# Kernel tuning notes

Measured on AMD Instinct MI355X. Metric: run time of the kernel, lower is better.

The kernel has to match this reference:

```python
import jax, jax.numpy as jnp
import numpy as np
from jax.scipy.special import logsumexp

B, S, L = 256, 512, 128


def setup_inputs() -> dict:
    key = jax.random.key(0)
    k1, k2, k3, k4, k5 = jax.random.split(key, 5)
    inputs = jax.random.normal(k1, (B, S, L), dtype=jnp.float32)
    labels = jax.random.randint(k2, (B, S), 0, L, dtype=jnp.int64)
    mask = jnp.ones((B, S), dtype=bool)
    # xavier_normal for (L, L): std = sqrt(2 / (L + L))
    transitions = jax.random.normal(k3, (L, L), dtype=jnp.float32) * np.sqrt(2.0 / (2 * L))
    start_transitions = jax.random.normal(k4, (L,), dtype=jnp.float32)
    end_transitions = jax.random.normal(k5, (L,), dtype=jnp.float32)
    return {
        "inputs": inputs,
        "labels": labels,
        "mask": mask,
        "transitions": transitions,
        "start_transitions": start_transitions,
        "end_transitions": end_transitions,
    }


def _input_likelihood(logits, transitions, start_t, end_t, mask):
    # logits: [B,S,L], mask: [B,S] bool -> logZ: [B]
    logits_t = jnp.swapaxes(logits, 0, 1)  # [S,B,L]
    mask_t = jnp.swapaxes(mask, 0, 1)      # [S,B]
    alpha0 = start_t[None, :] + logits_t[0]  # [B,L]

    def step(alpha, xs):
        emit, m = xs  # emit: [B,L], m: [B]
        # inner[b, i, j] = alpha[b,i] + emit[b,j] + T[i,j]
        inner = alpha[:, :, None] + emit[:, None, :] + transitions[None, :, :]
        new_alpha = logsumexp(inner, axis=1)  # [B,L]
        alpha = jnp.where(m[:, None], new_alpha, alpha)
        return alpha, None

    alpha, _ = jax.lax.scan(step, alpha0, (logits_t[1:], mask_t[1:]))
    stops = alpha + end_t[None, :]
    return logsumexp(stops, axis=-1)  # [B]


def _joint_likelihood(logits, transitions, start_t, end_t, tags, mask):
    # logits: [B,S,L], tags/mask: [B,S] -> score: [B]
    b, s, l = logits.shape
    maskf = mask.astype(logits.dtype)
    score = start_t[tags[:, 0]]  # [B]
    # transition scores for i = 0..S-2, gated by mask[:, i+1]
    trans_sc = transitions[tags[:, :-1], tags[:, 1:]] * maskf[:, 1:]  # [B,S-1]
    # emit scores at positions 0..S-2, gated by mask[:, i]
    emit_all = jnp.take_along_axis(logits, tags[:, :, None], axis=2)[:, :, 0]  # [B,S]
    emit_sc = emit_all[:, :-1] * maskf[:, :-1]
    score = score + trans_sc.sum(axis=1) + emit_sc.sum(axis=1)
    # last valid tag per sequence
    last_idx = mask.sum(axis=1).astype(jnp.int32) - 1  # [B]
    last_tags = jnp.take_along_axis(tags, last_idx[:, None], axis=1)[:, 0]  # [B]
    score = score + end_t[last_tags]
    last_input_sc = jnp.take_along_axis(logits[:, -1, :], last_tags[:, None], axis=1)[:, 0]
    score = score + last_input_sc * maskf[:, -1]
    return score


def reference(inputs, labels, mask, transitions, start_transitions, end_transitions):
    log_denominator = _input_likelihood(inputs, transitions, start_transitions, end_transitions, mask)
    log_numerator = _joint_likelihood(inputs, transitions, start_transitions, end_transitions, labels, mask)
    return jnp.sum(log_numerator - log_denominator)
```

## Files before the change

### kernel.cpp

```cpp
#include <hip/hip_runtime.h>
#include <hip/hip_bf16.h>

#define BB 256
#define SS 512
#define LL 128
#define MB 16
#define NCH 16
#define NSCAN (2 * NCH * 16)
#define CST 16
#define WUP 8

typedef __attribute__((ext_vector_type(8))) short bf16x8;
typedef __attribute__((ext_vector_type(4))) float f32x4;

__device__ __forceinline__ unsigned short f2bf(float x) {
    __hip_bfloat16 h = __float2bfloat16(x);
    return *reinterpret_cast<unsigned short*>(&h);
}
__device__ __forceinline__ float bf2f_lo(unsigned u) { return __uint_as_float(u << 16); }
__device__ __forceinline__ float wave_sum(float v) {
    #pragma unroll
    for (int off = 32; off > 0; off >>= 1)
        v += __shfl_xor(v, off);
    return v;
}
__device__ __forceinline__ unsigned umax2(unsigned a, unsigned b) { return a > b ? a : b; }
__device__ __forceinline__ unsigned packbf(float lo, float hi) {
    unsigned ua = __float_as_uint(hi) + 0x8000u;
    unsigned ub = __float_as_uint(lo) + 0x8000u;
    return __builtin_amdgcn_perm(ua, ub, 0x07060302u);
}

template<int DIR>
__device__ __forceinline__ void scan_dir(
    const float* __restrict__ lg,
    const float* __restrict__ trans,
    const float* __restrict__ bnd,
    const int ci, const int gb, const bool exact,
    const int w, const int q, const int r15,
    unsigned short (*e_lds)[MB][136],
    float* __restrict__ vF, float* __restrict__ wB,
    float* __restrict__ fsA, float* __restrict__ feA, int* __restrict__ sigA)
{
    const int snap_t  = (DIR == 1) ? CST * ci : 511 - CST * ci;
    const int t_begin = exact ? ((DIR == 1) ? 1 : 510) : (snap_t - (WUP - 1) * DIR);
    const int tinit   = t_begin - DIR;
    const int nwarm   = exact ? 0 : WUP;
    const int nmeas   = (ci == NCH - 1) ? (CST - 1) : CST;

    bf16x8 afrag[2][4];
    #pragma unroll
    for (int nt = 0; nt < 2; ++nt) {
        const int j = (w << 5) + nt * 16 + r15;
        #pragma unroll
        for (int kt = 0; kt < 4; ++kt) {
            const int k0 = kt * 32 + (q << 3);
            bf16x8 f;
            #pragma unroll
            for (int i = 0; i < 8; ++i) {
                const int k = k0 + i;
                const float tv = (DIR == 1) ? trans[k * LL + j] : trans[j * LL + k];
                ((unsigned short*)&f)[i] = f2bf(__expf(tv));
            }
            afrag[nt][kt] = f;
        }
    }

    bf16x8 bfrag[4];
    #pragma unroll
    for (int kt = 0; kt < 4; ++kt) {
        const int k0 = kt * 32 + (q << 3);
        bf16x8 f;
        #pragma unroll
        for (int i = 0; i < 8; ++i) {
            const int k = k0 + i;
            const float lv = lg[(size_t)tinit * LL + k];
            ((unsigned short*)&f)[i] = f2bf(__expf(exact ? (bnd[k] + lv) : lv));
        }
        bfrag[kt] = f;
    }

    const float* empf = lg + (w << 5) + (q << 2);
    auto ld2 = [&](int t, float4& a, float4& b) {
        int tp = t;
        tp = tp < 0 ? 0 : (tp > 511 ? 511 : tp);
        a = *(const float4*)(empf + (size_t)tp * LL);
        b = *(const float4*)(empf + (size_t)tp * LL + 16);
    };

    float4 e0a, e0b, e1a, e1b, e2a, e2b, e3a, e3b;
    ld2(t_begin,           e0a, e0b);
    ld2(t_begin + 1 * DIR, e1a, e1b);
    ld2(t_begin + 2 * DIR, e2a, e2b);
    ld2(t_begin + 3 * DIR, e3a, e3b);

    float scale_now = 1.0f, scale_nxt = 1.0f;
    int   pend_now  = 0,    pend_nxt  = 0;
    int   cexp      = 0;

    auto frag_sum = [&]() -> float {
        float s = 0.f;
        #pragma unroll
        for (int kt = 0; kt < 4; ++kt) {
            const unsigned short* pp = (const unsigned short*)&bfrag[kt];
            #pragma unroll
            for (int i = 0; i < 8; ++i)
                s += bf2f_lo((unsigned)pp[i]);
        }
        s += __shfl_xor(s, 16);
        s += __shfl_xor(s, 32);
        return s;
    };

    auto body = [&](int t, float4& ea, float4& eb) {
        float esc[8];
        esc[0] = scale_now * __expf(ea.x);
        esc[1] = scale_now * __expf(ea.y);
        esc[2] = scale_now * __expf(ea.z);
        esc[3] = scale_now * __expf(ea.w);
        esc[4] = scale_now * __expf(eb.x);
        esc[5] = scale_now * __expf(eb.y);
        esc[6] = scale_now * __expf(eb.z);
        esc[7] = scale_now * __expf(eb.w);
        f32x4 a0a = {0,0,0,0}, a0b = {0,0,0,0}, a1a = {0,0,0,0}, a1b = {0,0,0,0};
        a0a = __builtin_amdgcn_mfma_f32_16x16x32_bf16(afrag[0][0], bfrag[0], a0a, 0, 0, 0);
        a0b = __builtin_amdgcn_mfma_f32_16x16x32_bf16(afrag[0][1], bfrag[1], a0b, 0, 0, 0);
        a1a = __builtin_amdgcn_mfma_f32_16x16x32_bf16(afrag[1][0], bfrag[0], a1a, 0, 0, 0);
        a1b = __builtin_amdgcn_mfma_f32_16x16x32_bf16(afrag[1][1], bfrag[1], a1b, 0, 0, 0);
        a0a = __builtin_amdgcn_mfma_f32_16x16x32_bf16(afrag[0][2], bfrag[2], a0a, 0, 0, 0);
        a0b = __builtin_amdgcn_mfma_f32_16x16x32_bf16(afrag[0][3], bfrag[3], a0b, 0, 0, 0);
        a1a = __builtin_amdgcn_mfma_f32_16x16x32_bf16(afrag[1][2], bfrag[2], a1a, 0, 0, 0);
        a1b = __builtin_amdgcn_mfma_f32_16x16x32_bf16(afrag[1][3], bfrag[3], a1b, 0, 0, 0);
        cexp += pend_now;
        ld2(t + 4 * DIR, ea, eb);
        unsigned p[4];
        p[0] = packbf((a0a[0] + a0b[0]) * esc[0], (a0a[1] + a0b[1]) * esc[1]);
        p[1] = packbf((a0a[2] + a0b[2]) * esc[2], (a0a[3] + a0b[3]) * esc[3]);
        p[2] = packbf((a1a[0] + a1b[0]) * esc[4], (a1a[1] + a1b[1]) * esc[5]);
        p[3] = packbf((a1a[2] + a1b[2]) * esc[6], (a1a[3] + a1b[3]) * esc[7]);
        const int buf = t & 1;
        *(uint2*)&e_lds[buf][r15][(w << 5) + (q << 2)]      = make_uint2(p[0], p[1]);
        *(uint2*)&e_lds[buf][r15][(w << 5) + 16 + (q << 2)] = make_uint2(p[2], p[3]);
        asm volatile("s_waitcnt lgkmcnt(0)" ::: "memory");
        __builtin_amdgcn_s_barrier();
        asm volatile("" ::: "memory");
        unsigned um = 0u;
        #pragma unroll
        for (int kt = 0; kt < 4; ++kt) {
            bfrag[kt] = *(const bf16x8*)&e_lds[buf][r15][kt * 32 + (q << 3)];
            const unsigned* pu = (const unsigned*)&bfrag[kt];
            um = umax2(umax2(umax2(um, pu[0]), pu[1]), umax2(pu[2], pu[3]));
        }
        um = umax2(um, (unsigned)__shfl_xor((int)um, 16));
        um = umax2(um, (unsigned)__shfl_xor((int)um, 32));
        const int ke = (int)((um >> 23) & 0xff);
        scale_now = scale_nxt;
        pend_now  = pend_nxt;
        scale_nxt = __int_as_float((254 - ke) << 23);
        pend_nxt  = ke - 127;
    };

    int t = t_begin;
    for (int n = 0; n < nwarm; n += 4) {
        body(t,           e0a, e0b);
        body(t + 1 * DIR, e1a, e1b);
        body(t + 2 * DIR, e2a, e2b);
        body(t + 3 * DIR, e3a, e3b);
        t += 4 * DIR;
    }

    const float fs_val = frag_sum();
    cexp = 0;

    const int nm4 = nmeas & ~3;
    for (int n = 0; n < nm4; n += 4) {
        body(t,           e0a, e0b);
        body(t + 1 * DIR, e1a, e1b);
        body(t + 2 * DIR, e2a, e2b);
        body(t + 3 * DIR, e3a, e3b);
        t += 4 * DIR;
    }
    if (nm4 < nmeas) {
        body(t,           e0a, e0b);
        body(t + 1 * DIR, e1a, e1b);
        body(t + 2 * DIR, e2a, e2b);
    }

    const float fe_val = frag_sum();

    if (DIR == 1) {
        if (ci == NCH - 1 && w == 0) {
            #pragma unroll
            for (int kt = 0; kt < 4; ++kt) {
                const unsigned short* pp = (const unsigned short*)&bfrag[kt];
                float4 o0, o1;
                o0.x = bf2f_lo((unsigned)pp[0]); o0.y = bf2f_lo((unsigned)pp[1]);
                o0.z = bf2f_lo((unsigned)pp[2]); o0.w = bf2f_lo((unsigned)pp[3]);
                o1.x = bf2f_lo((unsigned)pp[4]); o1.y = bf2f_lo((unsigned)pp[5]);
                o1.z = bf2f_lo((unsigned)pp[6]); o1.w = bf2f_lo((unsigned)pp[7]);
                *(float4*)&vF[(size_t)gb * LL + kt * 32 + (q << 3)]     = o0;
                *(float4*)&vF[(size_t)gb * LL + kt * 32 + (q << 3) + 4] = o1;
            }
        }
    } else if (ci == NCH - 1) {
        f32x4 a0a = {0,0,0,0}, a0b = {0,0,0,0}, a1a = {0,0,0,0}, a1b = {0,0,0,0};
        a0a = __builtin_amdgcn_mfma_f32_16x16x32_bf16(afrag[0][0], bfrag[0], a0a, 0, 0, 0);
        a0b = __builtin_amdgcn_mfma_f32_16x16x32_bf16(afrag[0][1], bfrag[1], a0b, 0, 0, 0);
        a1a = __builtin_amdgcn_mfma_f32_16x16x32_bf16(afrag[1][0], bfrag[0], a1a, 0, 0, 0);
        a1b = __builtin_amdgcn_mfma_f32_16x16x32_bf16(afrag[1][1], bfrag[1], a1b, 0, 0, 0);
        a0a = __builtin_amdgcn_mfma_f32_16x16x32_bf16(afrag[0][2], bfrag[2], a0a, 0, 0, 0);
        a0b = __builtin_amdgcn_mfma_f32_16x16x32_bf16(afrag[0][3], bfrag[3], a0b, 0, 0, 0);
        a1a = __builtin_amdgcn_mfma_f32_16x16x32_bf16(afrag[1][2], bfrag[2], a1a, 0, 0, 0);
        a1b = __builtin_amdgcn_mfma_f32_16x16x32_bf16(afrag[1][3], bfrag[3], a1b, 0, 0, 0);
        float4 o0, o1;
        o0.x = a0a[0] + a0b[0]; o0.y = a0a[1] + a0b[1];
        o0.z = a0a[2] + a0b[2]; o0.w = a0a[3] + a0b[3];
        o1.x = a1a[0] + a1b[0]; o1.y = a1a[1] + a1b[1];
        o1.z = a1a[2] + a1b[2]; o1.w = a1a[3] + a1b[3];
        *(float4*)&wB[(size_t)gb * LL + (w << 5) + 0  + (q << 2)] = o0;
        *(float4*)&wB[(size_t)gb * LL + (w << 5) + 16 + (q << 2)] = o1;
    }

    const int slot = (DIR == 1) ? ci : ci + NCH;
    if (threadIdx.x < 16) {
        sigA[slot * BB + gb] = cexp;
        fsA [slot * BB + gb] = fs_val;
        feA [slot * BB + gb] = fe_val;
    }
}

__global__ __launch_bounds__(256) void crf_fb(
    const float* __restrict__ logits,
    const int*  __restrict__ labels,
    const float* __restrict__ trans,
    const float* __restrict__ start_t,
    const float* __restrict__ end_t,
    float* __restrict__ vF, float* __restrict__ wB,
    float* __restrict__ fsA, float* __restrict__ feA, int* __restrict__ sigA,
    float* __restrict__ out)
{
    const int tid  = threadIdx.x;
    const int w    = tid >> 6;
    const int lane = tid & 63;
    const int q    = lane >> 4;
    const int r15  = lane & 15;

    __shared__ unsigned short e_lds[2][MB][136];
    __shared__ float jred[4];

    const int slot = blockIdx.x >> 4;
    const int g    = blockIdx.x & 15;
    const bool bwd = (slot >= NCH);
    const int  ci  = bwd ? slot - NCH : slot;
    const int  gb  = g * MB + r15;
    const float* lg = logits + (size_t)gb * SS * LL;

    if (!bwd)
        scan_dir<1>(lg, trans, start_t, ci, gb, ci == 0, w, q, r15,
                    e_lds, vF, wB, fsA, feA, sigA);
    else
        scan_dir<-1>(lg, trans, end_t, ci, gb, ci == 0, w, q, r15,
                     e_lds, vF, wB, fsA, feA, sigA);

    {
        const int p  = blockIdx.x * 256 + tid;
        const int b  = p >> 9;
        const int t  = p & 511;
        const int* tg = labels + b * SS;
        const int tag = tg[t];
        float jacc = logits[(size_t)b * SS * LL + (size_t)t * LL + tag];
        if (t > 0)       jacc += trans[tg[t - 1] * LL + tag];
        else             jacc += start_t[tag];
        if (t == SS - 1) jacc += end_t[tag];
        jacc = wave_sum(jacc);
        if (lane == 0) jred[w] = jacc;
        __syncthreads();
        if (tid == 0) atomicAdd(out, jred[0] + jred[1] + jred[2] + jred[3]);
    }
}

__global__ __launch_bounds__(64) void crf_combine(
    const float* __restrict__ vF, const float* __restrict__ wB,
    const float* __restrict__ fsA, const float* __restrict__ feA,
    const int* __restrict__ sigA, float* __restrict__ out)
{
    const int b = blockIdx.x;
    const int lane = threadIdx.x;
    float d = vF[(size_t)b * LL + lane]      * wB[(size_t)b * LL + lane]
            + vF[(size_t)b * LL + 64 + lane] * wB[(size_t)b * LL + 64 + lane];
    const float dot = wave_sum(d);
    float term = 0.f;
    if (lane < 2 * NCH) {
        const int c = lane;
        term = (float)sigA[c * BB + b] * 0.6931471805599453f;
        if (c != NCH - 1 && c != 2 * NCH - 1) term += __logf(feA[c * BB + b]);
        if (c != 0 && c != NCH)               term -= __logf(fsA[c * BB + b]);
    }
    const float tsum = wave_sum(term);
    if (lane == 0) atomicAdd(out, -(tsum + __logf(dot)));
}

__global__ __launch_bounds__(256) void crf_forward_v3(
    const float* __restrict__ logits,
    const float* __restrict__ trans,
    const float* __restrict__ start_t,
    const float* __restrict__ end_t,
    float* __restrict__ out)
{
    const int tid  = threadIdx.x;
    const int w    = tid >> 6;
    const int lane = tid & 63;
    const int q    = lane >> 4;
    const int r15  = lane & 15;
    const int gb   = blockIdx.x * MB + r15;

    __shared__ unsigned short e_lds[2][MB][136];

    bf16x8 afrag[2][4];
    #pragma unroll
    for (int nt = 0; nt < 2; ++nt) {
        const int j = (w << 5) + nt * 16 + r15;
        #pragma unroll
        for (int kt = 0; kt < 4; ++kt) {
            const int k0 = kt * 32 + (q << 3);
            bf16x8 f;
            #pragma unroll
            for (int i = 0; i < 8; ++i)
                ((unsigned short*)&f)[i] = f2bf(__expf(trans[(k0 + i) * LL + j]));
            afrag[nt][kt] = f;
        }
    }

    const float* lgb = logits + (size_t)gb * (SS * LL);

    bf16x8 bfrag[4];
    #pragma unroll
    for (int kt = 0; kt < 4; ++kt) {
        const int k0 = kt * 32 + (q << 3);
        bf16x8 f;
        #pragma unroll
        for (int i = 0; i < 8; ++i)
            ((unsigned short*)&f)[i] = f2bf(__expf(start_t[k0 + i] + lgb[k0 + i]));
        bfrag[kt] = f;
    }

    const float* emp0 = lgb + (w << 5) + (q << 2);
    float4 emA0 = *(const float4*)(emp0 + 1 * LL);
    float4 emA1 = *(const float4*)(emp0 + 1 * LL + 16);
    float4 emB0 = *(const float4*)(emp0 + 2 * LL);
    float4 emB1 = *(const float4*)(emp0 + 2 * LL + 16);

    float scale = 1.0f;
    int   cexp  = 0;
    int   pend  = 0;

    auto body = [&](int t, float4& e0, float4& e1) {
        f32x4 acc0 = {0.f, 0.f, 0.f, 0.f};
        f32x4 acc1 = {0.f, 0.f, 0.f, 0.f};
        #pragma unroll
        for (int kt = 0; kt < 4; ++kt) {
            acc0 = __builtin_amdgcn_mfma_f32_16x16x32_bf16(afrag[0][kt], bfrag[kt], acc0, 0, 0, 0);
            acc1 = __builtin_amdgcn_mfma_f32_16x16x32_bf16(afrag[1][kt], bfrag[kt], acc1, 0, 0, 0);
        }
        cexp += pend;
        const float em[8] = {e0.x, e0.y, e0.z, e0.w, e1.x, e1.y, e1.z, e1.w};
        if (t + 2 < SS) {
            e0 = *(const float4*)(emp0 + (t + 2) * LL);
            e1 = *(const float4*)(emp0 + (t + 2) * LL + 16);
        }
        float vv[8];
        #pragma unroll
        for (int i = 0; i < 4; ++i) {
            vv[i]     = acc0[i] * scale * __expf(em[i]);
            vv[4 + i] = acc1[i] * scale * __expf(em[4 + i]);
        }
        unsigned p[4];
        #pragma unroll
        for (int i = 0; i < 4; ++i)
            p[i] = (unsigned)f2bf(vv[2 * i]) | ((unsigned)f2bf(vv[2 * i + 1]) << 16);
        const int buf = t & 1;
        *(uint2*)&e_lds[buf][r15][(w << 5) + (q << 2)]      = make_uint2(p[0], p[1]);
        *(uint2*)&e_lds[buf][r15][(w << 5) + 16 + (q << 2)] = make_uint2(p[2], p[3]);
        __syncthreads();
        unsigned umax = 0u;
        #pragma unroll
        for (int kt = 0; kt < 4; ++kt) {
            bfrag[kt] = *(const bf16x8*)&e_lds[buf][r15][kt * 32 + (q << 3)];
            const unsigned* pu = (const unsigned*)&bfrag[kt];
            umax = umax2(umax2(umax2(umax, pu[0]), pu[1]), umax2(pu[2], pu[3]));
        }
        umax = umax2(umax, (unsigned)__shfl_xor((int)umax, 16));
        umax = umax2(umax, (unsigned)__shfl_xor((int)umax, 32));
        const int ke = (int)((umax >> 23) & 0xff);
        scale = __int_as_float((254 - ke) << 23);
        pend  = ke - 127;
    };

    for (int t = 1; t + 1 < SS; t += 2) {
        body(t,     emA0, emA1);
        body(t + 1, emB0, emB1);
    }
    body(SS - 1, emA0, emA1);

    float s = 0.f;
    #pragma unroll
    for (int kt = 0; kt < 4; ++kt) {
        const int k0 = kt * 32 + (q << 3);
        const unsigned short* pp = (const unsigned short*)&bfrag[kt];
        #pragma unroll
        for (int i = 0; i < 8; ++i)
            s += bf2f_lo((unsigned)pp[i]) * __expf(end_t[k0 + i]);
    }
    s += __shfl_xor(s, 16);
    s += __shfl_xor(s, 32);
    if (tid < 16) {
        const float denom = (float)cexp * 0.6931471805599453f + __logf(s);
        atomicAdd(out, -denom);
    }
}

__global__ __launch_bounds__(64) void crf_joint(
    const float* __restrict__ logits,
    const int*  __restrict__ labels,
    const float* __restrict__ trans,
    const float* __restrict__ start_t,
    const float* __restrict__ end_t,
    float* __restrict__ out)
{
    const int b    = blockIdx.x;
    const int lane = threadIdx.x;
    const int*   tg  = labels + b * SS;
    const float* lgb = logits + (size_t)b * SS * LL;

    float acc = 0.f;
    for (int t = lane; t < SS; t += 64) {
        int tag = tg[t];
        acc += lgb[(size_t)t * LL + tag];
        if (t > 0) acc += trans[tg[t - 1] * LL + tag];
    }
    acc = wave_sum(acc);
    if (lane == 0) {
        acc += start_t[tg[0]] + end_t[tg[SS - 1]];
        atomicAdd(out, acc);
    }
}

extern "C" void kernel_launch(void* const* d_in, const int* in_sizes, int n_in,
                              void* d_out, int out_size, void* d_ws, size_t ws_size,
                              hipStream_t stream) {
    const float* inputs  = (const float*)d_in[0];
    const int*   labels  = (const int*)d_in[1];
    const float* trans   = (const float*)d_in[3];
    const float* start_t = (const float*)d_in[4];
    const float* end_t   = (const float*)d_in[5];
    float* out = (float*)d_out;

    const size_t vecB = (size_t)BB * LL * 4;
    const size_t scB  = (size_t)(2 * NCH) * BB * 4;
    const size_t need = 2 * vecB + 3 * scB;
    hipMemsetAsync(out, 0, sizeof(float), stream);

    if (ws_size >= need) {
        char* wsb = (char*)d_ws;
        float* vF  = (float*)wsb;
        float* wW  = (float*)(wsb + vecB);
        float* fsA = (float*)(wsb + 2 * vecB);
        float* feA = (float*)(wsb + 2 * vecB + scB);
        int*   sgA = (int*)  (wsb + 2 * vecB + 2 * scB);
        crf_fb<<<NSCAN, 256, 0, stream>>>(
            inputs, labels, trans, start_t, end_t, vF, wW, fsA, feA, sgA, out);
        crf_combine<<<BB, 64, 0, stream>>>(vF, wW, fsA, feA, sgA, out);
    } else {
        crf_forward_v3<<<(BB / MB), 256, 0, stream>>>(inputs, trans, start_t, end_t, out);
        crf_joint<<<BB, 64, 0, stream>>>(inputs, labels, trans, start_t, end_t, out);
    }
}
```

Measured before the change: 46.86 us.

## Run each chunk scan in a single wavefront to drop per-step block barriers

Each scan block shrinks from four wavefronts to one, so that wavefront now holds the full 128x128 transition fragment set and issues all 32 MFMAs per step. The per-step LDS exchange no longer needs s_barrier or double buffering, removing cross-wave synchronisation from the serial recurrence. In exchange each step's MFMA chain becomes four times longer on one SIMD, register pressure rises sharply (afrag[8][4] plus 16 float4 emission prefetches), and total active waves drop fourfold.

```diff
diff --git a/kernel.cpp b/kernel.cpp
--- a/kernel.cpp
+++ b/kernel.cpp
@@ -32,26 +32,32 @@
 }
 
 template<int DIR>
-__device__ __forceinline__ void scan_dir(
-    const float* __restrict__ lg,
+__device__ __forceinline__ void scan1w(
+    const float* __restrict__ logits,
     const float* __restrict__ trans,
     const float* __restrict__ bnd,
-    const int ci, const int gb, const bool exact,
-    const int w, const int q, const int r15,
-    unsigned short (*e_lds)[MB][136],
+    const int ci, const int g,
+    unsigned short* __restrict__ e_row,
     float* __restrict__ vF, float* __restrict__ wB,
     float* __restrict__ fsA, float* __restrict__ feA, int* __restrict__ sigA)
 {
+    const int lane = threadIdx.x;
+    const int q    = lane >> 4;
+    const int r15  = lane & 15;
+    const int gb   = g * MB + r15;
+    const float* lg = logits + (size_t)gb * SS * LL;
+    const bool exact = (ci == 0);
+
     const int snap_t  = (DIR == 1) ? CST * ci : 511 - CST * ci;
     const int t_begin = exact ? ((DIR == 1) ? 1 : 510) : (snap_t - (WUP - 1) * DIR);
     const int tinit   = t_begin - DIR;
     const int nwarm   = exact ? 0 : WUP;
     const int nmeas   = (ci == NCH - 1) ? (CST - 1) : CST;
 
-    bf16x8 afrag[2][4];
-    #pragma unroll
-    for (int nt = 0; nt < 2; ++nt) {
-        const int j = (w << 5) + nt * 16 + r15;
+    bf16x8 afrag[8][4];
+    #pragma unroll
+    for (int nt = 0; nt < 8; ++nt) {
+        const int j = nt * 16 + r15;
         #pragma unroll
         for (int kt = 0; kt < 4; ++kt) {
             const int k0 = kt * 32 + (q << 3);
@@ -80,19 +86,15 @@
         bfrag[kt] = f;
     }
 
-    const float* empf = lg + (w << 5) + (q << 2);
-    auto ld2 = [&](int t, float4& a, float4& b) {
-        int tp = t;
-        tp = tp < 0 ? 0 : (tp > 511 ? 511 : tp);
-        a = *(const float4*)(empf + (size_t)tp * LL);
-        b = *(const float4*)(empf + (size_t)tp * LL + 16);
+    auto ld8 = [&](int t, float4 (&d)[8]) {
+        int tc = t < 0 ? 0 : (t > 511 ? 511 : t);
+        #pragma unroll
+        for (int nt = 0; nt < 8; ++nt)
+            d[nt] = *(const float4*)(lg + (size_t)tc * LL + nt * 16 + (q << 2));
     };
-
-    float4 e0a, e0b, e1a, e1b, e2a, e2b, e3a, e3b;
-    ld2(t_begin,           e0a, e0b);
-    ld2(t_begin + 1 * DIR, e1a, e1b);
-    ld2(t_begin + 2 * DIR, e2a, e2b);
-    ld2(t_begin + 3 * DIR, e3a, e3b);
+    float4 emA[8], emB[8];
+    ld8(t_begin,       emA);
+    ld8(t_begin + DIR, emB);
 
     float scale_now = 1.0f, scale_nxt = 1.0f;
     int   pend_now  = 0,    pend_nxt  = 0;
@@ -112,42 +114,37 @@
         return s;
     };
 
-    auto body = [&](int t, float4& ea, float4& eb) {
-        float esc[8];
-        esc[0] = scale_now * __expf(ea.x);
-        esc[1] = scale_now * __expf(ea.y);
-        esc[2] = scale_now * __expf(ea.z);
-        esc[3] = scale_now * __expf(ea.w);
-        esc[4] = scale_now * __expf(eb.x);
-        esc[5] = scale_now * __expf(eb.y);
-        esc[6] = scale_now * __expf(eb.z);
-        esc[7] = scale_now * __expf(eb.w);
-        f32x4 a0a = {0,0,0,0}, a0b = {0,0,0,0}, a1a = {0,0,0,0}, a1b = {0,0,0,0};
-        a0a = __builtin_amdgcn_mfma_f32_16x16x32_bf16(afrag[0][0], bfrag[0], a0a, 0, 0, 0);
-        a0b = __builtin_amdgcn_mfma_f32_16x16x32_bf16(afrag[0][1], bfrag[1], a0b, 0, 0, 0);
-        a1a = __builtin_amdgcn_mfma_f32_16x16x32_bf16(afrag[1][0], bfrag[0], a1a, 0, 0, 0);
-        a1b = __builtin_amdgcn_mfma_f32_16x16x32_bf16(afrag[1][1], bfrag[1], a1b, 0, 0, 0);
-        a0a = __builtin_amdgcn_mfma_f32_16x16x32_bf16(afrag[0][2], bfrag[2], a0a, 0, 0, 0);
-        a0b = __builtin_amdgcn_mfma_f32_16x16x32_bf16(afrag[0][3], bfrag[3], a0b, 0, 0, 0);
-        a1a = __builtin_amdgcn_mfma_f32_16x16x32_bf16(afrag[1][2], bfrag[2], a1a, 0, 0, 0);
-        a1b = __builtin_amdgcn_mfma_f32_16x16x32_bf16(afrag[1][3], bfrag[3], a1b, 0, 0, 0);
+    auto body = [&](int t, float4 (&em)[8]) {
+        float esc[8][4];
+        #pragma unroll
+        for (int nt = 0; nt < 8; ++nt) {
+            esc[nt][0] = scale_now * __expf(em[nt].x);
+            esc[nt][1] = scale_now * __expf(em[nt].y);
+            esc[nt][2] = scale_now * __expf(em[nt].z);
+            esc[nt][3] = scale_now * __expf(em[nt].w);
+        }
+        f32x4 acc[8];
+        #pragma unroll
+        for (int nt = 0; nt < 8; ++nt) acc[nt] = (f32x4){0.f, 0.f, 0.f, 0.f};
+        #pragma unroll
+        for (int kt = 0; kt < 4; ++kt) {
+            #pragma unroll
+            for (int nt = 0; nt < 8; ++nt)
+                acc[nt] = __builtin_amdgcn_mfma_f32_16x16x32_bf16(
+                    afrag[nt][kt], bfrag[kt], acc[nt], 0, 0, 0);
+        }
         cexp += pend_now;
-        ld2(t + 4 * DIR, ea, eb);
-        unsigned p[4];
-        p[0] = packbf((a0a[0] + a0b[0]) * esc[0], (a0a[1] + a0b[1]) * esc[1]);
-        p[1] = packbf((a0a[2] + a0b[2]) * esc[2], (a0a[3] + a0b[3]) * esc[3]);
-        p[2] = packbf((a1a[0] + a1b[0]) * esc[4], (a1a[1] + a1b[1]) * esc[5]);
-        p[3] = packbf((a1a[2] + a1b[2]) * esc[6], (a1a[3] + a1b[3]) * esc[7]);
-        const int buf = t & 1;
-        *(uint2*)&e_lds[buf][r15][(w << 5) + (q << 2)]      = make_uint2(p[0], p[1]);
-        *(uint2*)&e_lds[buf][r15][(w << 5) + 16 + (q << 2)] = make_uint2(p[2], p[3]);
-        asm volatile("s_waitcnt lgkmcnt(0)" ::: "memory");
-        __builtin_amdgcn_s_barrier();
-        asm volatile("" ::: "memory");
+        ld8(t + 2 * DIR, em);
+        #pragma unroll
+        for (int nt = 0; nt < 8; ++nt) {
+            unsigned p0 = packbf(acc[nt][0] * esc[nt][0], acc[nt][1] * esc[nt][1]);
+            unsigned p1 = packbf(acc[nt][2] * esc[nt][2], acc[nt][3] * esc[nt][3]);
+            *(uint2*)&e_row[r15 * 136 + nt * 16 + (q << 2)] = make_uint2(p0, p1);
+        }
         unsigned um = 0u;
         #pragma unroll
         for (int kt = 0; kt < 4; ++kt) {
-            bfrag[kt] = *(const bf16x8*)&e_lds[buf][r15][kt * 32 + (q << 3)];
+            bfrag[kt] = *(const bf16x8*)&e_row[r15 * 136 + kt * 32 + (q << 3)];
             const unsigned* pu = (const unsigned*)&bfrag[kt];
             um = umax2(umax2(umax2(um, pu[0]), pu[1]), umax2(pu[2], pu[3]));
         }
@@ -161,35 +158,24 @@
     };
 
     int t = t_begin;
-    for (int n = 0; n < nwarm; n += 4) {
-        body(t,           e0a, e0b);
-        body(t + 1 * DIR, e1a, e1b);
-        body(t + 2 * DIR, e2a, e2b);
-        body(t + 3 * DIR, e3a, e3b);
-        t += 4 * DIR;
-    }
-
+    for (int n = 0; n < nwarm; n += 2) {
+        body(t,       emA);
+        body(t + DIR, emB);
+        t += 2 * DIR;
+    }
     const float fs_val = frag_sum();
     cexp = 0;
-
-    const int nm4 = nmeas & ~3;
-    for (int n = 0; n < nm4; n += 4) {
-        body(t,           e0a, e0b);
-        body(t + 1 * DIR, e1a, e1b);
-        body(t + 2 * DIR, e2a, e2b);
-        body(t + 3 * DIR, e3a, e3b);
-        t += 4 * DIR;
-    }
-    if (nm4 < nmeas) {
-        body(t,           e0a, e0b);
-        body(t + 1 * DIR, e1a, e1b);
-        body(t + 2 * DIR, e2a, e2b);
-    }
-
+    const int nm2 = nmeas & ~1;
+    for (int n = 0; n < nm2; n += 2) {
+        body(t,       emA);
+        body(t + DIR, emB);
+        t += 2 * DIR;
+    }
+    if (nm2 < nmeas) body(t, emA);
     const float fe_val = frag_sum();
 
     if (DIR == 1) {
-        if (ci == NCH - 1 && w == 0) {
+        if (ci == NCH - 1) {
             #pragma unroll
             for (int kt = 0; kt < 4; ++kt) {
                 const unsigned short* pp = (const unsigned short*)&bfrag[kt];
@@ -203,33 +189,33 @@
             }
         }
     } else if (ci == NCH - 1) {
-        f32x4 a0a = {0,0,0,0}, a0b = {0,0,0,0}, a1a = {0,0,0,0}, a1b = {0,0,0,0};
-        a0a = __builtin_amdgcn_mfma_f32_16x16x32_bf16(afrag[0][0], bfrag[0], a0a, 0, 0, 0);
-        a0b = __builtin_amdgcn_mfma_f32_16x16x32_bf16(afrag[0][1], bfrag[1], a0b, 0, 0, 0);
-        a1a = __builtin_amdgcn_mfma_f32_16x16x32_bf16(afrag[1][0], bfrag[0], a1a, 0, 0, 0);
-        a1b = __builtin_amdgcn_mfma_f32_16x16x32_bf16(afrag[1][1], bfrag[1], a1b, 0, 0, 0);
-        a0a = __builtin_amdgcn_mfma_f32_16x16x32_bf16(afrag[0][2], bfrag[2], a0a, 0, 0, 0);
-        a0b = __builtin_amdgcn_mfma_f32_16x16x32_bf16(afrag[0][3], bfrag[3], a0b, 0, 0, 0);
-        a1a = __builtin_amdgcn_mfma_f32_16x16x32_bf16(afrag[1][2], bfrag[2], a1a, 0, 0, 0);
-        a1b = __builtin_amdgcn_mfma_f32_16x16x32_bf16(afrag[1][3], bfrag[3], a1b, 0, 0, 0);
-        float4 o0, o1;
-        o0.x = a0a[0] + a0b[0]; o0.y = a0a[1] + a0b[1];
-        o0.z = a0a[2] + a0b[2]; o0.w = a0a[3] + a0b[3];
-        o1.x = a1a[0] + a1b[0]; o1.y = a1a[1] + a1b[1];
-        o1.z = a1a[2] + a1b[2]; o1.w = a1a[3] + a1b[3];
-        *(float4*)&wB[(size_t)gb * LL + (w << 5) + 0  + (q << 2)] = o0;
-        *(float4*)&wB[(size_t)gb * LL + (w << 5) + 16 + (q << 2)] = o1;
+        f32x4 acc[8];
+        #pragma unroll
+        for (int nt = 0; nt < 8; ++nt) acc[nt] = (f32x4){0.f, 0.f, 0.f, 0.f};
+        #pragma unroll
+        for (int kt = 0; kt < 4; ++kt) {
+            #pragma unroll
+            for (int nt = 0; nt < 8; ++nt)
+                acc[nt] = __builtin_amdgcn_mfma_f32_16x16x32_bf16(
+                    afrag[nt][kt], bfrag[kt], acc[nt], 0, 0, 0);
+        }
+        #pragma unroll
+        for (int nt = 0; nt < 8; ++nt) {
+            float4 o;
+            o.x = acc[nt][0]; o.y = acc[nt][1]; o.z = acc[nt][2]; o.w = acc[nt][3];
+            *(float4*)&wB[(size_t)gb * LL + nt * 16 + (q << 2)] = o;
+        }
     }
 
     const int slot = (DIR == 1) ? ci : ci + NCH;
-    if (threadIdx.x < 16) {
+    if (lane < 16) {
         sigA[slot * BB + gb] = cexp;
         fsA [slot * BB + gb] = fs_val;
         feA [slot * BB + gb] = fe_val;
     }
 }
 
-__global__ __launch_bounds__(256) void crf_fb(
+__global__ __launch_bounds__(64, 1) void crf_fb(
     const float* __restrict__ logits,
     const int*  __restrict__ labels,
     const float* __restrict__ trans,
@@ -239,43 +225,35 @@
     float* __restrict__ fsA, float* __restrict__ feA, int* __restrict__ sigA,
     float* __restrict__ out)
 {
-    const int tid  = threadIdx.x;
-    const int w    = tid >> 6;
-    const int lane = tid & 63;
-    const int q    = lane >> 4;
-    const int r15  = lane & 15;
-
-    __shared__ unsigned short e_lds[2][MB][136];
-    __shared__ float jred[4];
+    const int lane = threadIdx.x;
+    __shared__ unsigned short e_row[MB * 136];
 
     const int slot = blockIdx.x >> 4;
     const int g    = blockIdx.x & 15;
     const bool bwd = (slot >= NCH);
     const int  ci  = bwd ? slot - NCH : slot;
-    const int  gb  = g * MB + r15;
-    const float* lg = logits + (size_t)gb * SS * LL;
 
     if (!bwd)
-        scan_dir<1>(lg, trans, start_t, ci, gb, ci == 0, w, q, r15,
-                    e_lds, vF, wB, fsA, feA, sigA);
+        scan1w<1>(logits, trans, start_t, ci, g, e_row, vF, wB, fsA, feA, sigA);
     else
-        scan_dir<-1>(lg, trans, end_t, ci, gb, ci == 0, w, q, r15,
-                     e_lds, vF, wB, fsA, feA, sigA);
+        scan1w<-1>(logits, trans, end_t, ci, g, e_row, vF, wB, fsA, feA, sigA);
 
     {
-        const int p  = blockIdx.x * 256 + tid;
-        const int b  = p >> 9;
-        const int t  = p & 511;
-        const int* tg = labels + b * SS;
-        const int tag = tg[t];
-        float jacc = logits[(size_t)b * SS * LL + (size_t)t * LL + tag];
-        if (t > 0)       jacc += trans[tg[t - 1] * LL + tag];
-        else             jacc += start_t[tag];
-        if (t == SS - 1) jacc += end_t[tag];
+        float jacc = 0.f;
+        #pragma unroll
+        for (int u = 0; u < 4; ++u) {
+            const int p = blockIdx.x * 256 + u * 64 + lane;
+            const int b = p >> 9;
+            const int t = p & 511;
+            const int* tg = labels + b * SS;
+            const int tag = tg[t];
+            jacc += logits[(size_t)b * SS * LL + (size_t)t * LL + tag];
+            if (t > 0)       jacc += trans[tg[t - 1] * LL + tag];
+            else             jacc += start_t[tag];
+            if (t == SS - 1) jacc += end_t[tag];
+        }
         jacc = wave_sum(jacc);
-        if (lane == 0) jred[w] = jacc;
-        __syncthreads();
-        if (tid == 0) atomicAdd(out, jred[0] + jred[1] + jred[2] + jred[3]);
+        if (lane == 0) atomicAdd(out, jacc);
     }
 }
 
@@ -467,7 +445,7 @@
         float* fsA = (float*)(wsb + 2 * vecB);
         float* feA = (float*)(wsb + 2 * vecB + scB);
         int*   sgA = (int*)  (wsb + 2 * vecB + 2 * scB);
-        crf_fb<<<NSCAN, 256, 0, stream>>>(
+        crf_fb<<<NSCAN, 64, 0, stream>>>(
             inputs, labels, trans, start_t, end_t, vF, wW, fsA, feA, sgA, out);
         crf_combine<<<BB, 64, 0, stream>>>(vF, wW, fsA, feA, sgA, out);
     } else {
```

Result: slower. 50.69 us (+8.2%).
